# Optimization experiments

Measured on AMD Instinct MI355X. Metric: run time of the kernel, lower is better.

## Reference

```python
import jax, jax.numpy as jnp
import numpy as np

B, T, C, H = 2, 2048, 1024, 16
D = C // H  # head_dim = 64


def wheel_softmax(scores):
    """Wheel-arithmetic softmax: total division, bot (0/0) positions -> 0.
    Rows that are entirely -inf yield sum==0 -> bot -> filled with 0.0,
    matching wheel_out.to_numpy_safe(bot_fill=0.0, inf_fill=0.0)."""
    m = jnp.max(scores, axis=-1, keepdims=True)
    safe_m = jnp.where(jnp.isfinite(m), m, 0.0)
    e = jnp.exp(scores - safe_m)          # -inf entries -> 0
    z = jnp.sum(e, axis=-1, keepdims=True)
    ok = z > 0
    return jnp.where(ok, e / jnp.where(ok, z, 1.0), 0.0)


def setup_inputs() -> dict:
    key = jax.random.key(0)
    ks = jax.random.split(key, 12)
    s = 1.0 / np.sqrt(C)
    inp = {
        "query": jax.random.normal(ks[0], (B, T, C), jnp.float32),
        "key": jax.random.normal(ks[1], (B, T, C), jnp.float32),
        "value": jax.random.normal(ks[2], (B, T, C), jnp.float32),
        "q_w": jax.random.normal(ks[3], (C, C), jnp.float32) * s,
        "q_b": jax.random.normal(ks[4], (C,), jnp.float32) * 0.01,
        "k_w": jax.random.normal(ks[5], (C, C), jnp.float32) * s,
        "k_b": jax.random.normal(ks[6], (C,), jnp.float32) * 0.01,
        "v_w": jax.random.normal(ks[7], (C, C), jnp.float32) * s,
        "v_b": jax.random.normal(ks[8], (C,), jnp.float32) * 0.01,
        "o_w": jax.random.normal(ks[9], (C, C), jnp.float32) * s,
        "o_b": jax.random.normal(ks[10], (C,), jnp.float32) * 0.01,
        "key_padding_mask": jax.random.randint(ks[11], (B, T), 0, 2).astype(bool),
    }
    return inp


def reference(query, key, value, q_w, q_b, k_w, k_b, v_w, v_b, o_w, o_b, key_padding_mask):
    scale = D ** -0.5
    def proj(x, w, b):
        # nn.Linear: x @ w.T + b ; reshape to [B,H,T,D]
        y = jnp.einsum("btc,oc->bto", x, w) + b
        return y.reshape(B, T, H, D).transpose(0, 2, 1, 3)
    Q = proj(query, q_w, q_b)
    K = proj(key, k_w, k_b)
    V = proj(value, v_w, v_b)
    scores = jnp.einsum("bhqd,bhkd->bhqk", Q, K) * scale
    scores = jnp.where(key_padding_mask[:, None, None, :], -jnp.inf, scores)
    weights = wheel_softmax(scores)  # dropout=0 -> identity
    out = jnp.einsum("bhqk,bhkd->bhqd", weights, V)
    out = out.transpose(0, 2, 1, 3).reshape(B, T, C)
    out = jnp.einsum("btc,oc->bto", out, o_w) + o_b
    return (out, weights)
```

## Files before the change

kernel.cpp:

```cpp
#include <hip/hip_runtime.h>
#include <math.h>


typedef _Float16 f16;
typedef _Float16 f16x2 __attribute__((ext_vector_type(2)));
typedef _Float16 f16x4 __attribute__((ext_vector_type(4)));
typedef _Float16 f16x8 __attribute__((ext_vector_type(8)));
typedef float  f32x2  __attribute__((ext_vector_type(2)));
typedef float  f32x4  __attribute__((ext_vector_type(4)));

#define MFMAH(a, b, c)  __builtin_amdgcn_mfma_f32_16x16x32_f16((a), (b), (c), 0, 0, 0)

__device__ __forceinline__ void gload16(void* lds, const void* g) {
  __builtin_amdgcn_global_load_lds((__attribute__((address_space(1))) void*)(g),
                                   (__attribute__((address_space(3))) void*)(lds),
                                   16, 0, 0);
}

__global__ __launch_bounds__(256) void conv_f16(const float* __restrict__ q, const float* __restrict__ k,
                                                const float* __restrict__ v, const float* __restrict__ qw,
                                                const float* __restrict__ kw, const float* __restrict__ vw,
                                                const float* __restrict__ ow, f16* __restrict__ xf) {
  long long i = ((long long)blockIdx.x * 256 + threadIdx.x) * 4;
  const float* src;
  long long off;
  if (i < 4194304)       { src = q;  off = 0; }
  else if (i < 8388608)  { src = k;  off = 4194304; }
  else if (i < 12582912) { src = v;  off = 8388608; }
  else if (i < 13631488) { src = qw; off = 12582912; }
  else if (i < 14680064) { src = kw; off = 13631488; }
  else if (i < 15728640) { src = vw; off = 14680064; }
  else                   { src = ow; off = 15728640; }
  f32x4 val = *(const f32x4*)(src + (i - off));
  f16x4 h;
#pragma unroll
  for (int r = 0; r < 4; ++r) h[r] = (f16)val[r];
  *(f16x4*)(xf + i) = h;
}

__device__ __forceinline__ void stage64(f16* lds, const f16* g, int row0, int kc, int tid) {
#pragma unroll
  for (int j = 0; j < 4; ++j) {
    int chunk = j * 256 + tid;
    int r = chunk >> 3, cpos = chunk & 7;
    int csrc = cpos ^ (r & 7);
    gload16((char*)lds + chunk * 16,
            (const char*)(g + (size_t)(row0 + r) * 1024 + kc) + csrc * 16);
  }
}

__device__ __forceinline__ f16x8 frag64(const f16* lds, int row, int c) {
  int pos = c ^ (row & 7);
  return *(const f16x8*)((const char*)lds + row * 128 + pos * 16);
}

__device__ __forceinline__ void gemm_core(const f16* A, const f16* X, int o0, int t0, int tid,
                                          f16* sA, f16* sB, f32x4 acc[4][4]) {
  int wid = tid >> 6, lane = tid & 63;
  int wm = wid >> 1, wn = wid & 1, g = lane >> 4, r15 = lane & 15;
  for (int kc = 0; kc < 1024; kc += 64) {
    __syncthreads();
    stage64(sA, A, o0, kc, tid);
    stage64(sB, X, t0, kc, tid);
    __syncthreads();
    f16x8 a0[4], a1[4], x0[4], x1[4];
#pragma unroll
    for (int f = 0; f < 4; ++f) {
      int ra = wm * 64 + f * 16 + r15;
      int rx = wn * 64 + f * 16 + r15;
      a0[f] = frag64(sA, ra, g);
      a1[f] = frag64(sA, ra, 4 + g);
      x0[f] = frag64(sB, rx, g);
      x1[f] = frag64(sB, rx, 4 + g);
    }
#pragma unroll
    for (int fm = 0; fm < 4; ++fm)
#pragma unroll
      for (int fn = 0; fn < 4; ++fn) {
        acc[fm][fn] = MFMAH(a0[fm], x0[fn], acc[fm][fn]);
        acc[fm][fn] = MFMAH(a1[fm], x1[fn], acc[fm][fn]);
      }
  }
}

__global__ __launch_bounds__(256, 3) void gemm_qkv(const f16* __restrict__ xf,
                                                   const float* __restrict__ q_b, const float* __restrict__ k_b,
                                                   const float* __restrict__ v_b,
                                                   f16* __restrict__ Qf, f16* __restrict__ Kf,
                                                   f16* __restrict__ VT2) {
  __shared__ f16 sA[8192], sB[8192];
  int z = blockIdx.z;
  int tid = threadIdx.x;
  int wid = tid >> 6, lane = tid & 63;
  int wm = wid >> 1, wn = wid & 1, g = lane >> 4, r15 = lane & 15;
  f32x4 acc[4][4] = {};
  if (z == 2) {
    const f16* X = xf + 8388608;
    const f16* W = xf + 14680064;
    int o0 = blockIdx.x * 128, t0 = blockIdx.y * 128;
    gemm_core(X, W, t0, o0, tid, sA, sB, acc);
#pragma unroll
    for (int fm = 0; fm < 4; ++fm)
#pragma unroll
      for (int fn = 0; fn < 4; ++fn) {
        int tb = t0 + wm * 64 + fm * 16 + 4 * g;
        int o  = o0 + wn * 64 + fn * 16 + r15;
        int bb = tb >> 11, tl = tb & 2047, hh = o >> 6, dd = o & 63;
        int ch = tl >> 5, c = tl & 31;
        int slotbase = (c < 16) ? ((c >> 2) << 3) : ((((c - 16) >> 2) << 3) + 4);
        float bo = v_b[o];
        f16x4 v4;
#pragma unroll
        for (int r = 0; r < 4; ++r) v4[r] = (f16)(acc[fm][fn][r] + bo);
        *(f16x4*)(VT2 + ((((size_t)bb * 16 + hh) * 64 + ch) * 64 + dd) * 32 + slotbase) = v4;
      }
  } else {
    const f16* A = xf + (z ? 13631488 : 12582912);
    const f16* X = xf + (z ? 4194304 : 0);
    const float* bias = z ? k_b : q_b;
    f16* Yf = z ? Kf : Qf;
    float scale = z ? 1.0f : 0.125f;
    int o0 = blockIdx.x * 128, t0 = blockIdx.y * 128;
    gemm_core(A, X, o0, t0, tid, sA, sB, acc);
#pragma unroll
    for (int fm = 0; fm < 4; ++fm)
#pragma unroll
      for (int fn = 0; fn < 4; ++fn) {
        int ob = o0 + wm * 64 + fm * 16 + 4 * g;
        int t  = t0 + wn * 64 + fn * 16 + r15;
        int bb = t >> 11, tl = t & 2047, hh = ob >> 6, dd = ob & 63;
        size_t base = (((size_t)bb * 16 + hh) * 2048 + tl) * 64 + dd;
        f16x4 vh;
#pragma unroll
        for (int r = 0; r < 4; ++r)
          vh[r] = (f16)((acc[fm][fn][r] + bias[ob + r]) * scale);
        *(f16x4*)(Yf + base) = vh;
      }
  }
}

__global__ __launch_bounds__(256, 3) void gemm_o(const f16* __restrict__ xf, const f16* __restrict__ Abuf,
                                                 const float* __restrict__ o_b, float* __restrict__ OutF) {
  __shared__ f16 sA[8192], sB[8192];
  const f16* A = xf + 15728640;
  int tid = threadIdx.x;
  int o0 = blockIdx.x * 128, t0 = blockIdx.y * 128;
  int wid = tid >> 6, lane = tid & 63;
  int wm = wid >> 1, wn = wid & 1, g = lane >> 4, r15 = lane & 15;
  f32x4 acc[4][4] = {};
  gemm_core(A, Abuf, o0, t0, tid, sA, sB, acc);
#pragma unroll
  for (int fm = 0; fm < 4; ++fm)
#pragma unroll
    for (int fn = 0; fn < 4; ++fn) {
      int ob = o0 + wm * 64 + fm * 16 + 4 * g;
      int t  = t0 + wn * 64 + fn * 16 + r15;
      f32x4 v;
#pragma unroll
      for (int r = 0; r < 4; ++r) v[r] = acc[fm][fn][r] + o_b[ob + r];
      *(f32x4*)(OutF + (size_t)t * 1024 + ob) = v;
    }
}

__global__ __launch_bounds__(512, 6) void attn_kernel(
    const f16* __restrict__ Qf, const f16* __restrict__ Kf,
    const f16* __restrict__ VT2, const int* __restrict__ mask,
    float* __restrict__ wout, f16* __restrict__ Abuf) {
  __shared__ char smemA[8][4224];
  __shared__ f16 pvh[8][16][72];
  __shared__ float ps[128];
  __shared__ float rz[16];
  int tid = threadIdx.x;
  int wid = tid >> 6, lane = tid & 63;
  int g = lane >> 4, r15 = lane & 15;
  int bid = blockIdx.x;
  int swz = (bid & 7) * 512 + (bid >> 3);
  int qt = swz & 127, bh = swz >> 7;
  int b = bh >> 4, h = bh & 15;
  int q0 = qt * 16;

  const f16* qp = Qf + ((size_t)bh * 2048 + q0 + r15) * 64 + 8 * g;
  f16x8 qh0 = *(const f16x8*)(qp);
  f16x8 qh1 = *(const f16x8*)(qp + 32);

  const int* mp = mask + b * 2048 + wid * 256 + 4 * g;
  unsigned long long mb = 0;
#pragma unroll
  for (int t = 0; t < 16; ++t) {
    int4 ma = *(const int4*)(mp + t * 16);
    mb |= ((ma.x ? 1ull : 0ull) << (4 * t)) | ((ma.y ? 1ull : 0ull) << (4 * t + 1)) |
          ((ma.z ? 1ull : 0ull) << (4 * t + 2)) | ((ma.w ? 1ull : 0ull) << (4 * t + 3));
  }

  f16* kb0 = (f16*)&smemA[wid][0];
  f16* kb1 = (f16*)&smemA[wid][2048];
  const f16* ksrcA = Kf + ((size_t)bh * 2048 + wid * 256 + (lane >> 3)) * 64 +
                     (((lane & 7) ^ ((lane >> 3) & 7)) * 8);
  const f16* ksrcB = ksrcA + 8 * 64;

  gload16(kb0, ksrcA);
  gload16(kb0 + 512, ksrcB);
  gload16(kb1, ksrcA + 1024);
  gload16(kb1 + 512, ksrcB + 1024);
  asm volatile("s_waitcnt vmcnt(2)" ::: "memory");
  int key = r15 & 7;
  f16x8 c0 = *(const f16x8*)(kb0 + r15 * 64 + ((g ^ key) * 8));
  f16x8 c1 = *(const f16x8*)(kb0 + r15 * 64 + (((g + 4) ^ key) * 8));

  float psum = 0.f;
  f16x4 p16[16];
#pragma unroll
  for (int s = 0; s < 16; ++s) {
    if (s < 14) {
      asm volatile("s_waitcnt lgkmcnt(0)" ::: "memory");
      f16* nb = (s & 1) ? kb1 : kb0;
      gload16(nb, ksrcA + (s + 2) * 1024);
      gload16(nb + 512, ksrcB + (s + 2) * 1024);
    }
    f16x8 n0, n1;
    if (s < 15) {
      if (s < 14) asm volatile("s_waitcnt vmcnt(2)" ::: "memory");
      else        asm volatile("s_waitcnt vmcnt(0)" ::: "memory");
      const f16* nt = ((s + 1) & 1) ? kb1 : kb0;
      n0 = *(const f16x8*)(nt + r15 * 64 + ((g ^ key) * 8));
      n1 = *(const f16x8*)(nt + r15 * 64 + (((g + 4) ^ key) * 8));
    }
    f32x4 sc = {0.f, 0.f, 0.f, 0.f};
    sc = MFMAH(c0, qh0, sc);
    sc = MFMAH(c1, qh1, sc);
    f16x4 pk;
#pragma unroll
    for (int r = 0; r < 4; ++r) {
      float e = ((mb >> (4 * s + r)) & 1) ? 0.f : __expf(sc[r]);
      psum += e;
      pk[r] = (f16)e;
    }
    p16[s] = pk;
    c0 = n0;
    c1 = n1;
  }

  psum += __shfl_xor(psum, 16);
  psum += __shfl_xor(psum, 32);
  if (lane < 16) ps[lane * 8 + wid] = psum;
  __syncthreads();

  if (tid < 128) {
    float z = ps[tid];
#pragma unroll
    for (int m = 1; m <= 4; m <<= 1) z += __shfl_xor(z, m);
    if ((tid & 7) == 0) rz[tid >> 3] = (z > 0.f) ? 1.0f / z : 0.0f;
  }
  __syncthreads();

  f32x4 acc[4] = {};
  {
    char* pst = &smemA[wid][0];
    int c5 = lane & 31, hi5 = lane >> 5;
    float* wrowbase = wout + ((size_t)bh * 2048 + q0) * 2048 + wid * 256;
    const f16* vb = VT2 + (((size_t)bh * 64 + wid * 8) * 64 + r15) * 32 + g * 8;
    f16x8 v0 = *(const f16x8*)(vb);
    f16x8 v1 = *(const f16x8*)(vb + 512);
    f16x8 v2 = *(const f16x8*)(vb + 1024);
    f16x8 v3 = *(const f16x8*)(vb + 1536);
#pragma unroll
    for (int t = 0; t < 8; ++t) {
      f16x8 n0, n1, n2, n3;
      if (t < 7) {
        const f16* nvb = vb + (t + 1) * 2048;
        n0 = *(const f16x8*)(nvb);
        n1 = *(const f16x8*)(nvb + 512);
        n2 = *(const f16x8*)(nvb + 1024);
        n3 = *(const f16x8*)(nvb + 1536);
      }
      if (t == 0 || t == 4) {
        int hb = (t >> 2) * 8;
#pragma unroll
        for (int s2 = 0; s2 < 8; ++s2)
          *(f16x4*)(pst + r15 * 264 + s2 * 32 + g * 8) = p16[hb + s2];
        asm volatile("s_waitcnt lgkmcnt(0)" ::: "memory");
      }
      {
        int hh2 = t >> 2, rbase = (t & 3) * 4;
#pragma unroll
        for (int u = 0; u < 2; ++u) {
          int row = rbase + 2 * u + hi5;
          f16x4 pv4 = *(const f16x4*)(pst + row * 264 + c5 * 8);
          float rzr = rz[row];
          f32x4 wv;
#pragma unroll
          for (int r = 0; r < 4; ++r) wv[r] = (float)pv4[r] * rzr;
          __builtin_nontemporal_store(wv,
              (f32x4*)(wrowbase + (size_t)row * 2048 + hh2 * 128 + 4 * c5));
        }
      }
      f16x8 af = __builtin_shufflevector(p16[2 * t], p16[2 * t + 1], 0, 1, 2, 3, 4, 5, 6, 7);
      acc[0] = MFMAH(af, v0, acc[0]);
      acc[1] = MFMAH(af, v1, acc[1]);
      acc[2] = MFMAH(af, v2, acc[2]);
      acc[3] = MFMAH(af, v3, acc[3]);
      v0 = n0; v1 = n1; v2 = n2; v3 = n3;
    }
#pragma unroll
    for (int dt = 0; dt < 4; ++dt)
#pragma unroll
      for (int r = 0; r < 4; ++r)
        pvh[wid][4 * g + r][dt * 16 + r15] = (f16)acc[dt][r];
  }
  __syncthreads();

  {
    int q = tid >> 5, d = (tid & 31) * 2;
    float a0 = 0.f, a1 = 0.f;
#pragma unroll
    for (int w8 = 0; w8 < 8; ++w8) {
      f16x2 v = *(const f16x2*)&pvh[w8][q][d];
      a0 += (float)v[0];
      a1 += (float)v[1];
    }
    float rzq = rz[q];
    f16x2 o2 = {(f16)(a0 * rzq), (f16)(a1 * rzq)};
    *(f16x2*)(Abuf + ((size_t)b * 2048 + q0 + q) * 1024 + h * 64 + d) = o2;
  }
}

extern "C" void kernel_launch(void* const* d_in, const int* in_sizes, int n_in,
                              void* d_out, int out_size, void* d_ws, size_t ws_size,
                              hipStream_t stream) {
  const float* query = (const float*)d_in[0];
  const float* key_i = (const float*)d_in[1];
  const float* value = (const float*)d_in[2];
  const float* q_w = (const float*)d_in[3];
  const float* q_b = (const float*)d_in[4];
  const float* k_w = (const float*)d_in[5];
  const float* k_b = (const float*)d_in[6];
  const float* v_w = (const float*)d_in[7];
  const float* v_b = (const float*)d_in[8];
  const float* o_w = (const float*)d_in[9];
  const float* o_b = (const float*)d_in[10];
  const int* mask = (const int*)d_in[11];
  float* out = (float*)d_out;
  float* wout = out + 4194304;

  const size_t XFB = 16777216ull * 2;
  const size_t QB = 4194304ull * 2;
  if (ws_size < XFB + 4 * QB) return;
  f16* xf   = (f16*)d_ws;
  f16* Qf   = (f16*)((char*)d_ws + XFB);
  f16* Kf   = (f16*)((char*)d_ws + XFB + QB);
  f16* VT2  = (f16*)((char*)d_ws + XFB + 2 * QB);
  f16* Abuf = (f16*)((char*)d_ws + XFB + 3 * QB);

  conv_f16<<<16384, 256, 0, stream>>>(query, key_i, value, q_w, k_w, v_w, o_w, xf);
  gemm_qkv<<<dim3(8, 32, 3), 256, 0, stream>>>(xf, q_b, k_b, v_b, Qf, Kf, VT2);
  attn_kernel<<<4096, 512, 0, stream>>>(Qf, Kf, VT2, mask, wout, Abuf);
  gemm_o<<<dim3(8, 32), 256, 0, stream>>>(xf, Abuf, o_b, out);
}
```

Before: 247.6 us.

## Process two 16-row query tiles per attention block to reuse K/V loads

The attention kernel now handles 32 query rows per block (two 16-row MFMA tiles), so each K tile loaded into LDS and each V fragment read from global memory serves twice as many queries. The grid is halved and the launch bound drops from 6 to 4 blocks per CU. The weight-row stores no longer stage probabilities through LDS; each lane writes its own fp16 probabilities, scaled to fp32, straight to global memory. In exchange the kernel holds twice as many probability registers (two 16-entry p16 arrays), which raises register pressure and lowers occupancy, and the direct stores are less coalesced than the staged ones.

```diff
diff --git a/kernel.cpp b/kernel.cpp
--- a/kernel.cpp
+++ b/kernel.cpp
@@ -162,26 +162,73 @@
     }
 }
 
-__global__ __launch_bounds__(512, 6) void attn_kernel(
+#define PV_GROUP(P, RZV, WB, ROWOFF)                                          \
+  {                                                                           \
+    f32x4 acc0 = {}, acc1 = {}, acc2 = {}, acc3 = {};                         \
+    const f16* vb = VT2 + (((size_t)bh * 64 + wid * 8) * 64 + r15) * 32 + g * 8; \
+    f16x8 v0 = *(const f16x8*)(vb);                                           \
+    f16x8 v1 = *(const f16x8*)(vb + 512);                                     \
+    f16x8 v2 = *(const f16x8*)(vb + 1024);                                    \
+    f16x8 v3 = *(const f16x8*)(vb + 1536);                                    \
+    _Pragma("unroll")                                                         \
+    for (int t = 0; t < 8; ++t) {                                             \
+      f16x8 n0, n1, n2, n3;                                                   \
+      if (t < 7) {                                                            \
+        const f16* nvb = vb + (t + 1) * 2048;                                 \
+        n0 = *(const f16x8*)(nvb);                                            \
+        n1 = *(const f16x8*)(nvb + 512);                                      \
+        n2 = *(const f16x8*)(nvb + 1024);                                     \
+        n3 = *(const f16x8*)(nvb + 1536);                                     \
+      }                                                                       \
+      _Pragma("unroll")                                                       \
+      for (int u = 0; u < 2; ++u) {                                           \
+        int s = 2 * t + u;                                                    \
+        f16x4 pk = P[s];                                                      \
+        f32x4 wv;                                                             \
+        _Pragma("unroll")                                                     \
+        for (int r = 0; r < 4; ++r) wv[r] = (float)pk[r] * (RZV);             \
+        __builtin_nontemporal_store(wv, (f32x4*)((WB) + s * 16));             \
+      }                                                                       \
+      f16x8 af = __builtin_shufflevector(P[2 * t], P[2 * t + 1],              \
+                                         0, 1, 2, 3, 4, 5, 6, 7);             \
+      acc0 = MFMAH(af, v0, acc0);                                             \
+      acc1 = MFMAH(af, v1, acc1);                                             \
+      acc2 = MFMAH(af, v2, acc2);                                             \
+      acc3 = MFMAH(af, v3, acc3);                                             \
+      v0 = n0; v1 = n1; v2 = n2; v3 = n3;                                     \
+    }                                                                         \
+    f16* pvw = (f16*)(smemU + wid * 4352);                                    \
+    _Pragma("unroll")                                                         \
+    for (int r = 0; r < 4; ++r) {                                             \
+      pvw[((ROWOFF) + 4 * g + r) * 68 + 0 * 16 + r15] = (f16)acc0[r];         \
+      pvw[((ROWOFF) + 4 * g + r) * 68 + 1 * 16 + r15] = (f16)acc1[r];         \
+      pvw[((ROWOFF) + 4 * g + r) * 68 + 2 * 16 + r15] = (f16)acc2[r];         \
+      pvw[((ROWOFF) + 4 * g + r) * 68 + 3 * 16 + r15] = (f16)acc3[r];         \
+    }                                                                         \
+  }
+
+__global__ __launch_bounds__(512, 4) void attn_kernel(
     const f16* __restrict__ Qf, const f16* __restrict__ Kf,
     const f16* __restrict__ VT2, const int* __restrict__ mask,
     float* __restrict__ wout, f16* __restrict__ Abuf) {
-  __shared__ char smemA[8][4224];
-  __shared__ f16 pvh[8][16][72];
-  __shared__ float ps[128];
-  __shared__ float rz[16];
+  __shared__ char smemU[35072];
+  __shared__ float ps[256];
+  __shared__ float rz[32];
   int tid = threadIdx.x;
   int wid = tid >> 6, lane = tid & 63;
   int g = lane >> 4, r15 = lane & 15;
   int bid = blockIdx.x;
-  int swz = (bid & 7) * 512 + (bid >> 3);
-  int qt = swz & 127, bh = swz >> 7;
+  int swz = (bid & 7) * 256 + (bid >> 3);
+  int qt = swz & 63, bh = swz >> 6;
   int b = bh >> 4, h = bh & 15;
-  int q0 = qt * 16;
-
-  const f16* qp = Qf + ((size_t)bh * 2048 + q0 + r15) * 64 + 8 * g;
-  f16x8 qh0 = *(const f16x8*)(qp);
-  f16x8 qh1 = *(const f16x8*)(qp + 32);
+  int q0 = qt * 32;
+
+  const f16* qpa = Qf + ((size_t)bh * 2048 + q0 + r15) * 64 + 8 * g;
+  const f16* qpb = qpa + 16 * 64;
+  f16x8 qa0 = *(const f16x8*)(qpa);
+  f16x8 qa1 = *(const f16x8*)(qpa + 32);
+  f16x8 qb0 = *(const f16x8*)(qpb);
+  f16x8 qb1 = *(const f16x8*)(qpb + 32);
 
   const int* mp = mask + b * 2048 + wid * 256 + 4 * g;
   unsigned long long mb = 0;
@@ -192,11 +239,11 @@
           ((ma.z ? 1ull : 0ull) << (4 * t + 2)) | ((ma.w ? 1ull : 0ull) << (4 * t + 3));
   }
 
-  f16* kb0 = (f16*)&smemA[wid][0];
-  f16* kb1 = (f16*)&smemA[wid][2048];
+  f16* kb0 = (f16*)(smemU + wid * 4224);
+  f16* kb1 = kb0 + 1024;
   const f16* ksrcA = Kf + ((size_t)bh * 2048 + wid * 256 + (lane >> 3)) * 64 +
                      (((lane & 7) ^ ((lane >> 3) & 7)) * 8);
-  const f16* ksrcB = ksrcA + 8 * 64;
+  const f16* ksrcB = ksrcA + 512;
 
   gload16(kb0, ksrcA);
   gload16(kb0 + 512, ksrcB);
@@ -207,8 +254,8 @@
   f16x8 c0 = *(const f16x8*)(kb0 + r15 * 64 + ((g ^ key) * 8));
   f16x8 c1 = *(const f16x8*)(kb0 + r15 * 64 + (((g + 4) ^ key) * 8));
 
-  float psum = 0.f;
-  f16x4 p16[16];
+  float psa = 0.f, psb = 0.f;
+  f16x4 p16a[16], p16b[16];
 #pragma unroll
   for (int s = 0; s < 16; ++s) {
     if (s < 14) {
@@ -225,27 +272,39 @@
       n0 = *(const f16x8*)(nt + r15 * 64 + ((g ^ key) * 8));
       n1 = *(const f16x8*)(nt + r15 * 64 + (((g + 4) ^ key) * 8));
     }
-    f32x4 sc = {0.f, 0.f, 0.f, 0.f};
-    sc = MFMAH(c0, qh0, sc);
-    sc = MFMAH(c1, qh1, sc);
-    f16x4 pk;
+    f32x4 sa = {0.f, 0.f, 0.f, 0.f}, sb = {0.f, 0.f, 0.f, 0.f};
+    sa = MFMAH(c0, qa0, sa);
+    sb = MFMAH(c0, qb0, sb);
+    sa = MFMAH(c1, qa1, sa);
+    sb = MFMAH(c1, qb1, sb);
+    f16x4 pka, pkb;
 #pragma unroll
     for (int r = 0; r < 4; ++r) {
-      float e = ((mb >> (4 * s + r)) & 1) ? 0.f : __expf(sc[r]);
-      psum += e;
-      pk[r] = (f16)e;
-    }
-    p16[s] = pk;
+      int mkd = (mb >> (4 * s + r)) & 1;
+      float ea = mkd ? 0.f : __expf(sa[r]);
+      float eb = mkd ? 0.f : __expf(sb[r]);
+      psa += ea;
+      psb += eb;
+      pka[r] = (f16)ea;
+      pkb[r] = (f16)eb;
+    }
+    p16a[s] = pka;
+    p16b[s] = pkb;
     c0 = n0;
     c1 = n1;
   }
 
-  psum += __shfl_xor(psum, 16);
-  psum += __shfl_xor(psum, 32);
-  if (lane < 16) ps[lane * 8 + wid] = psum;
+  psa += __shfl_xor(psa, 16);
+  psa += __shfl_xor(psa, 32);
+  psb += __shfl_xor(psb, 16);
+  psb += __shfl_xor(psb, 32);
+  if (lane < 16) {
+    ps[r15 * 8 + wid] = psa;
+    ps[(16 + r15) * 8 + wid] = psb;
+  }
   __syncthreads();
 
-  if (tid < 128) {
+  if (tid < 256) {
     float z = ps[tid];
 #pragma unroll
     for (int m = 1; m <= 4; m <<= 1) z += __shfl_xor(z, m);
@@ -253,74 +312,25 @@
   }
   __syncthreads();
 
-  f32x4 acc[4] = {};
+  float rza = rz[r15];
+  float rzb = rz[16 + r15];
+  float* wba = wout + ((size_t)bh * 2048 + q0 + r15) * 2048 + wid * 256 + 4 * g;
+  float* wbb = wba + (size_t)16 * 2048;
+  PV_GROUP(p16a, rza, wba, 0)
+  PV_GROUP(p16b, rzb, wbb, 16)
+  __syncthreads();
+
   {
-    char* pst = &smemA[wid][0];
-    int c5 = lane & 31, hi5 = lane >> 5;
-    float* wrowbase = wout + ((size_t)bh * 2048 + q0) * 2048 + wid * 256;
-    const f16* vb = VT2 + (((size_t)bh * 64 + wid * 8) * 64 + r15) * 32 + g * 8;
-    f16x8 v0 = *(const f16x8*)(vb);
-    f16x8 v1 = *(const f16x8*)(vb + 512);
-    f16x8 v2 = *(const f16x8*)(vb + 1024);
-    f16x8 v3 = *(const f16x8*)(vb + 1536);
-#pragma unroll
-    for (int t = 0; t < 8; ++t) {
-      f16x8 n0, n1, n2, n3;
-      if (t < 7) {
-        const f16* nvb = vb + (t + 1) * 2048;
-        n0 = *(const f16x8*)(nvb);
-        n1 = *(const f16x8*)(nvb + 512);
-        n2 = *(const f16x8*)(nvb + 1024);
-        n3 = *(const f16x8*)(nvb + 1536);
-      }
-      if (t == 0 || t == 4) {
-        int hb = (t >> 2) * 8;
-#pragma unroll
-        for (int s2 = 0; s2 < 8; ++s2)
-          *(f16x4*)(pst + r15 * 264 + s2 * 32 + g * 8) = p16[hb + s2];
-        asm volatile("s_waitcnt lgkmcnt(0)" ::: "memory");
-      }
-      {
-        int hh2 = t >> 2, rbase = (t & 3) * 4;
-#pragma unroll
-        for (int u = 0; u < 2; ++u) {
-          int row = rbase + 2 * u + hi5;
-          f16x4 pv4 = *(const f16x4*)(pst + row * 264 + c5 * 8);
-          float rzr = rz[row];
-          f32x4 wv;
-#pragma unroll
-          for (int r = 0; r < 4; ++r) wv[r] = (float)pv4[r] * rzr;
-          __builtin_nontemporal_store(wv,
-              (f32x4*)(wrowbase + (size_t)row * 2048 + hh2 * 128 + 4 * c5));
-        }
-      }
-      f16x8 af = __builtin_shufflevector(p16[2 * t], p16[2 * t + 1], 0, 1, 2, 3, 4, 5, 6, 7);
-      acc[0] = MFMAH(af, v0, acc[0]);
-      acc[1] = MFMAH(af, v1, acc[1]);
-      acc[2] = MFMAH(af, v2, acc[2]);
-      acc[3] = MFMAH(af, v3, acc[3]);
-      v0 = n0; v1 = n1; v2 = n2; v3 = n3;
-    }
-#pragma unroll
-    for (int dt = 0; dt < 4; ++dt)
-#pragma unroll
-      for (int r = 0; r < 4; ++r)
-        pvh[wid][4 * g + r][dt * 16 + r15] = (f16)acc[dt][r];
-  }
-  __syncthreads();
-
-  {
-    int q = tid >> 5, d = (tid & 31) * 2;
-    float a0 = 0.f, a1 = 0.f;
+    int q = tid >> 4, d4 = (tid & 15) * 4;
+    float a0 = 0.f, a1 = 0.f, a2 = 0.f, a3 = 0.f;
 #pragma unroll
     for (int w8 = 0; w8 < 8; ++w8) {
-      f16x2 v = *(const f16x2*)&pvh[w8][q][d];
-      a0 += (float)v[0];
-      a1 += (float)v[1];
+      f16x4 v = *(const f16x4*)((const f16*)(smemU + w8 * 4352) + q * 68 + d4);
+      a0 += (float)v[0]; a1 += (float)v[1]; a2 += (float)v[2]; a3 += (float)v[3];
     }
     float rzq = rz[q];
-    f16x2 o2 = {(f16)(a0 * rzq), (f16)(a1 * rzq)};
-    *(f16x2*)(Abuf + ((size_t)b * 2048 + q0 + q) * 1024 + h * 64 + d) = o2;
+    f16x4 o4 = {(f16)(a0 * rzq), (f16)(a1 * rzq), (f16)(a2 * rzq), (f16)(a3 * rzq)};
+    *(f16x4*)(Abuf + ((size_t)b * 2048 + q0 + q) * 1024 + h * 64 + d4) = o4;
   }
 }
 
@@ -353,6 +363,6 @@
 
   conv_f16<<<16384, 256, 0, stream>>>(query, key_i, value, q_w, k_w, v_w, o_w, xf);
   gemm_qkv<<<dim3(8, 32, 3), 256, 0, stream>>>(xf, q_b, k_b, v_b, Qf, Kf, VT2);
-  attn_kernel<<<4096, 512, 0, stream>>>(Qf, Kf, VT2, mask, wout, Abuf);
+  attn_kernel<<<2048, 512, 0, stream>>>(Qf, Kf, VT2, mask, wout, Abuf);
   gemm_o<<<dim3(8, 32), 256, 0, stream>>>(xf, Abuf, o_b, out);
 }
```

Measured after the change: 328.3 us. +32.6%, slower.

## Give each wave a full query tile with a two-pass recompute of QK^T

Applied to the files above, without the earlier changes.

The attention kernel now assigns one 16-query tile per wave instead of splitting the keys across 8 waves of a block. A first pass computes only the softmax denominators. A second pass recomputes the scores, writes normalized weights and accumulates P·V, so the cross-wave LDS reductions and block barriers go away. In exchange the QK^T MFMAs and K/mask loads run twice, and K is read directly from global memory rather than through LDS double-buffering. Launch shape and occupancy hints change to 256 threads with fewer LDS bytes.

```diff
diff --git a/kernel.cpp b/kernel.cpp
--- a/kernel.cpp
+++ b/kernel.cpp
@@ -162,20 +162,19 @@
     }
 }
 
-__global__ __launch_bounds__(512, 6) void attn_kernel(
+__global__ __launch_bounds__(256, 5) void attn_kernel(
     const f16* __restrict__ Qf, const f16* __restrict__ Kf,
     const f16* __restrict__ VT2, const int* __restrict__ mask,
     float* __restrict__ wout, f16* __restrict__ Abuf) {
-  __shared__ char smemA[8][4224];
-  __shared__ f16 pvh[8][16][72];
-  __shared__ float ps[128];
-  __shared__ float rz[16];
+  __shared__ char pstage[4][4224];
   int tid = threadIdx.x;
   int wid = tid >> 6, lane = tid & 63;
   int g = lane >> 4, r15 = lane & 15;
+  int c5 = lane & 31, hi5 = lane >> 5;
   int bid = blockIdx.x;
-  int swz = (bid & 7) * 512 + (bid >> 3);
-  int qt = swz & 127, bh = swz >> 7;
+  int bswz = (bid & 7) * 128 + (bid >> 3);
+  int task = bswz * 4 + wid;
+  int qt = task & 127, bh = task >> 7;
   int b = bh >> 4, h = bh & 15;
   int q0 = qt * 16;
 
@@ -183,144 +182,123 @@
   f16x8 qh0 = *(const f16x8*)(qp);
   f16x8 qh1 = *(const f16x8*)(qp + 32);
 
-  const int* mp = mask + b * 2048 + wid * 256 + 4 * g;
-  unsigned long long mb = 0;
-#pragma unroll
-  for (int t = 0; t < 16; ++t) {
-    int4 ma = *(const int4*)(mp + t * 16);
-    mb |= ((ma.x ? 1ull : 0ull) << (4 * t)) | ((ma.y ? 1ull : 0ull) << (4 * t + 1)) |
-          ((ma.z ? 1ull : 0ull) << (4 * t + 2)) | ((ma.w ? 1ull : 0ull) << (4 * t + 3));
-  }
-
-  f16* kb0 = (f16*)&smemA[wid][0];
-  f16* kb1 = (f16*)&smemA[wid][2048];
-  const f16* ksrcA = Kf + ((size_t)bh * 2048 + wid * 256 + (lane >> 3)) * 64 +
-                     (((lane & 7) ^ ((lane >> 3) & 7)) * 8);
-  const f16* ksrcB = ksrcA + 8 * 64;
-
-  gload16(kb0, ksrcA);
-  gload16(kb0 + 512, ksrcB);
-  gload16(kb1, ksrcA + 1024);
-  gload16(kb1 + 512, ksrcB + 1024);
-  asm volatile("s_waitcnt vmcnt(2)" ::: "memory");
-  int key = r15 & 7;
-  f16x8 c0 = *(const f16x8*)(kb0 + r15 * 64 + ((g ^ key) * 8));
-  f16x8 c1 = *(const f16x8*)(kb0 + r15 * 64 + (((g + 4) ^ key) * 8));
+  const f16* kbase = Kf + ((size_t)bh * 2048 + r15) * 64 + 8 * g;
+  const int* mp = mask + b * 2048 + 4 * g;
 
   float psum = 0.f;
-  f16x4 p16[16];
-#pragma unroll
-  for (int s = 0; s < 16; ++s) {
-    if (s < 14) {
-      asm volatile("s_waitcnt lgkmcnt(0)" ::: "memory");
-      f16* nb = (s & 1) ? kb1 : kb0;
-      gload16(nb, ksrcA + (s + 2) * 1024);
-      gload16(nb + 512, ksrcB + (s + 2) * 1024);
-    }
-    f16x8 n0, n1;
-    if (s < 15) {
-      if (s < 14) asm volatile("s_waitcnt vmcnt(2)" ::: "memory");
-      else        asm volatile("s_waitcnt vmcnt(0)" ::: "memory");
-      const f16* nt = ((s + 1) & 1) ? kb1 : kb0;
-      n0 = *(const f16x8*)(nt + r15 * 64 + ((g ^ key) * 8));
-      n1 = *(const f16x8*)(nt + r15 * 64 + (((g + 4) ^ key) * 8));
-    }
-    f32x4 sc = {0.f, 0.f, 0.f, 0.f};
-    sc = MFMAH(c0, qh0, sc);
-    sc = MFMAH(c1, qh1, sc);
-    f16x4 pk;
-#pragma unroll
-    for (int r = 0; r < 4; ++r) {
-      float e = ((mb >> (4 * s + r)) & 1) ? 0.f : __expf(sc[r]);
-      psum += e;
-      pk[r] = (f16)e;
-    }
-    p16[s] = pk;
-    c0 = n0;
-    c1 = n1;
-  }
-
+  f16x8 a0 = *(const f16x8*)(kbase);
+  f16x8 a1 = *(const f16x8*)(kbase + 32);
+  f16x8 b0 = *(const f16x8*)(kbase + 1024);
+  f16x8 b1 = *(const f16x8*)(kbase + 1024 + 32);
+  int4 m0 = *(const int4*)(mp);
+  int4 m1 = *(const int4*)(mp + 16);
+  for (int s2 = 0; s2 < 64; ++s2) {
+    int sn = (s2 < 63) ? (2 * s2 + 2) : 126;
+    f16x8 na0 = *(const f16x8*)(kbase + (size_t)sn * 1024);
+    f16x8 na1 = *(const f16x8*)(kbase + (size_t)sn * 1024 + 32);
+    f16x8 nb0 = *(const f16x8*)(kbase + (size_t)(sn + 1) * 1024);
+    f16x8 nb1 = *(const f16x8*)(kbase + (size_t)(sn + 1) * 1024 + 32);
+    int4 nm0 = *(const int4*)(mp + sn * 16);
+    int4 nm1 = *(const int4*)(mp + (sn + 1) * 16);
+    f32x4 s0v = {0.f, 0.f, 0.f, 0.f}, s1v = {0.f, 0.f, 0.f, 0.f};
+    s0v = MFMAH(a0, qh0, s0v);
+    s1v = MFMAH(b0, qh0, s1v);
+    s0v = MFMAH(a1, qh1, s0v);
+    s1v = MFMAH(b1, qh1, s1v);
+    psum += (m0.x ? 0.f : __expf(s0v[0])) + (m0.y ? 0.f : __expf(s0v[1])) +
+            (m0.z ? 0.f : __expf(s0v[2])) + (m0.w ? 0.f : __expf(s0v[3]));
+    psum += (m1.x ? 0.f : __expf(s1v[0])) + (m1.y ? 0.f : __expf(s1v[1])) +
+            (m1.z ? 0.f : __expf(s1v[2])) + (m1.w ? 0.f : __expf(s1v[3]));
+    a0 = na0; a1 = na1; b0 = nb0; b1 = nb1;
+    m0 = nm0; m1 = nm1;
+  }
   psum += __shfl_xor(psum, 16);
   psum += __shfl_xor(psum, 32);
-  if (lane < 16) ps[lane * 8 + wid] = psum;
-  __syncthreads();
-
-  if (tid < 128) {
-    float z = ps[tid];
-#pragma unroll
-    for (int m = 1; m <= 4; m <<= 1) z += __shfl_xor(z, m);
-    if ((tid & 7) == 0) rz[tid >> 3] = (z > 0.f) ? 1.0f / z : 0.0f;
-  }
-  __syncthreads();
-
-  f32x4 acc[4] = {};
+  float rzv = (psum > 0.f) ? 1.0f / psum : 0.0f;
+  float rr[8];
+#pragma unroll
+  for (int i = 0; i < 8; ++i) rr[i] = __shfl(rzv, 2 * i + hi5);
+  float rq0 = __shfl(rzv, 4 * g + 0);
+  float rq1 = __shfl(rzv, 4 * g + 1);
+  float rq2 = __shfl(rzv, 4 * g + 2);
+  float rq3 = __shfl(rzv, 4 * g + 3);
+
+  char* pst = &pstage[wid][0];
+  float* wrow = wout + ((size_t)bh * 2048 + q0) * 2048;
+  const f16* vbase = VT2 + ((size_t)bh * 64 * 64 + r15) * 32 + g * 8;
+  f32x4 acc0 = {}, acc1 = {}, acc2 = {}, acc3 = {};
+
+  for (int grp = 0; grp < 16; ++grp) {
+    int s0 = grp * 8;
+    f16x4 P8[8];
+    f16x8 ka0 = *(const f16x8*)(kbase + (size_t)s0 * 1024);
+    f16x8 ka1 = *(const f16x8*)(kbase + (size_t)s0 * 1024 + 32);
+    int4 km = *(const int4*)(mp + s0 * 16);
+#pragma unroll
+    for (int t8 = 0; t8 < 8; ++t8) {
+      int s = s0 + t8;
+      int sn = (s < 127) ? (s + 1) : 127;
+      f16x8 na0 = *(const f16x8*)(kbase + (size_t)sn * 1024);
+      f16x8 na1 = *(const f16x8*)(kbase + (size_t)sn * 1024 + 32);
+      int4 nm = *(const int4*)(mp + sn * 16);
+      f32x4 sc = {0.f, 0.f, 0.f, 0.f};
+      sc = MFMAH(ka0, qh0, sc);
+      sc = MFMAH(ka1, qh1, sc);
+      f16x4 pk;
+      pk[0] = (f16)(km.x ? 0.f : __expf(sc[0]));
+      pk[1] = (f16)(km.y ? 0.f : __expf(sc[1]));
+      pk[2] = (f16)(km.z ? 0.f : __expf(sc[2]));
+      pk[3] = (f16)(km.w ? 0.f : __expf(sc[3]));
+      P8[t8] = pk;
+      ka0 = na0; ka1 = na1; km = nm;
+    }
+#pragma unroll
+    for (int t8 = 0; t8 < 8; ++t8)
+      *(f16x4*)(pst + r15 * 264 + t8 * 32 + g * 8) = P8[t8];
+    asm volatile("s_waitcnt lgkmcnt(0)" ::: "memory");
+#pragma unroll
+    for (int i = 0; i < 8; ++i) {
+      int row = 2 * i + hi5;
+      f16x4 pv4 = *(const f16x4*)(pst + row * 264 + c5 * 8);
+      f32x4 wv;
+#pragma unroll
+      for (int r = 0; r < 4; ++r) wv[r] = (float)pv4[r] * rr[i];
+      __builtin_nontemporal_store(wv,
+          (f32x4*)(wrow + (size_t)row * 2048 + grp * 128 + 4 * c5));
+    }
+#pragma unroll
+    for (int p = 0; p < 4; ++p) {
+      const f16* vb = vbase + (size_t)(grp * 4 + p) * 2048;
+      f16x8 v0 = *(const f16x8*)(vb);
+      f16x8 v1 = *(const f16x8*)(vb + 512);
+      f16x8 v2 = *(const f16x8*)(vb + 1024);
+      f16x8 v3 = *(const f16x8*)(vb + 1536);
+      f16x8 af = __builtin_shufflevector(P8[2 * p], P8[2 * p + 1], 0, 1, 2, 3, 4, 5, 6, 7);
+      acc0 = MFMAH(af, v0, acc0);
+      acc1 = MFMAH(af, v1, acc1);
+      acc2 = MFMAH(af, v2, acc2);
+      acc3 = MFMAH(af, v3, acc3);
+    }
+  }
+
   {
-    char* pst = &smemA[wid][0];
-    int c5 = lane & 31, hi5 = lane >> 5;
-    float* wrowbase = wout + ((size_t)bh * 2048 + q0) * 2048 + wid * 256;
-    const f16* vb = VT2 + (((size_t)bh * 64 + wid * 8) * 64 + r15) * 32 + g * 8;
-    f16x8 v0 = *(const f16x8*)(vb);
-    f16x8 v1 = *(const f16x8*)(vb + 512);
-    f16x8 v2 = *(const f16x8*)(vb + 1024);
-    f16x8 v3 = *(const f16x8*)(vb + 1536);
-#pragma unroll
-    for (int t = 0; t < 8; ++t) {
-      f16x8 n0, n1, n2, n3;
-      if (t < 7) {
-        const f16* nvb = vb + (t + 1) * 2048;
-        n0 = *(const f16x8*)(nvb);
-        n1 = *(const f16x8*)(nvb + 512);
-        n2 = *(const f16x8*)(nvb + 1024);
-        n3 = *(const f16x8*)(nvb + 1536);
-      }
-      if (t == 0 || t == 4) {
-        int hb = (t >> 2) * 8;
-#pragma unroll
-        for (int s2 = 0; s2 < 8; ++s2)
-          *(f16x4*)(pst + r15 * 264 + s2 * 32 + g * 8) = p16[hb + s2];
-        asm volatile("s_waitcnt lgkmcnt(0)" ::: "memory");
-      }
-      {
-        int hh2 = t >> 2, rbase = (t & 3) * 4;
-#pragma unroll
-        for (int u = 0; u < 2; ++u) {
-          int row = rbase + 2 * u + hi5;
-          f16x4 pv4 = *(const f16x4*)(pst + row * 264 + c5 * 8);
-          float rzr = rz[row];
-          f32x4 wv;
-#pragma unroll
-          for (int r = 0; r < 4; ++r) wv[r] = (float)pv4[r] * rzr;
-          __builtin_nontemporal_store(wv,
-              (f32x4*)(wrowbase + (size_t)row * 2048 + hh2 * 128 + 4 * c5));
-        }
-      }
-      f16x8 af = __builtin_shufflevector(p16[2 * t], p16[2 * t + 1], 0, 1, 2, 3, 4, 5, 6, 7);
-      acc[0] = MFMAH(af, v0, acc[0]);
-      acc[1] = MFMAH(af, v1, acc[1]);
-      acc[2] = MFMAH(af, v2, acc[2]);
-      acc[3] = MFMAH(af, v3, acc[3]);
-      v0 = n0; v1 = n1; v2 = n2; v3 = n3;
-    }
-#pragma unroll
-    for (int dt = 0; dt < 4; ++dt)
-#pragma unroll
-      for (int r = 0; r < 4; ++r)
-        pvh[wid][4 * g + r][dt * 16 + r15] = (f16)acc[dt][r];
-  }
-  __syncthreads();
-
-  {
-    int q = tid >> 5, d = (tid & 31) * 2;
-    float a0 = 0.f, a1 = 0.f;
-#pragma unroll
-    for (int w8 = 0; w8 < 8; ++w8) {
-      f16x2 v = *(const f16x2*)&pvh[w8][q][d];
-      a0 += (float)v[0];
-      a1 += (float)v[1];
-    }
-    float rzq = rz[q];
-    f16x2 o2 = {(f16)(a0 * rzq), (f16)(a1 * rzq)};
-    *(f16x2*)(Abuf + ((size_t)b * 2048 + q0 + q) * 1024 + h * 64 + d) = o2;
+    f16* ab = Abuf + ((size_t)b * 2048 + q0 + 4 * g) * 1024 + h * 64 + r15;
+    ab[0 * 1024 + 0]  = (f16)(acc0[0] * rq0);
+    ab[0 * 1024 + 16] = (f16)(acc1[0] * rq0);
+    ab[0 * 1024 + 32] = (f16)(acc2[0] * rq0);
+    ab[0 * 1024 + 48] = (f16)(acc3[0] * rq0);
+    ab[1 * 1024 + 0]  = (f16)(acc0[1] * rq1);
+    ab[1 * 1024 + 16] = (f16)(acc1[1] * rq1);
+    ab[1 * 1024 + 32] = (f16)(acc2[1] * rq1);
+    ab[1 * 1024 + 48] = (f16)(acc3[1] * rq1);
+    ab[2 * 1024 + 0]  = (f16)(acc0[2] * rq2);
+    ab[2 * 1024 + 16] = (f16)(acc1[2] * rq2);
+    ab[2 * 1024 + 32] = (f16)(acc2[2] * rq2);
+    ab[2 * 1024 + 48] = (f16)(acc3[2] * rq2);
+    ab[3 * 1024 + 0]  = (f16)(acc0[3] * rq3);
+    ab[3 * 1024 + 16] = (f16)(acc1[3] * rq3);
+    ab[3 * 1024 + 32] = (f16)(acc2[3] * rq3);
+    ab[3 * 1024 + 48] = (f16)(acc3[3] * rq3);
   }
 }
 
@@ -353,6 +331,6 @@
 
   conv_f16<<<16384, 256, 0, stream>>>(query, key_i, value, q_w, k_w, v_w, o_w, xf);
   gemm_qkv<<<dim3(8, 32, 3), 256, 0, stream>>>(xf, q_b, k_b, v_b, Qf, Kf, VT2);
-  attn_kernel<<<4096, 512, 0, stream>>>(Qf, Kf, VT2, mask, wout, Abuf);
+  attn_kernel<<<1024, 256, 0, stream>>>(Qf, Kf, VT2, mask, wout, Abuf);
   gemm_o<<<dim3(8, 32), 256, 0, stream>>>(xf, Abuf, o_b, out);
 }
```

Result: slower. 456.7 us (+84.4%).
